# Kernel optimization log

Hardware: AMD Instinct MI355X
Metric: run time of the kernel (lower is better)

Reference implementation:

```python
import jax, jax.numpy as jnp
import numpy as np

N_NODES = 50000
N_EDGES = 800000
NFEAT, NHID, NCLASS = 256, 64, 2


def _deg_norm(idx, n_nodes, dtype):
    deg = jax.ops.segment_sum(jnp.ones(idx.shape[0], dtype=dtype), idx, num_segments=n_nodes)
    return jax.lax.rsqrt(jnp.maximum(deg, 1.0))


def gcn_layer(x, W, b, src, dst, n_nodes):
    # DGL GraphConv, norm='both': h = D_in^{-1/2} * Agg( D_out^{-1/2} * x ) W + b
    # weight applied before aggregation (in_feats >= out_feats path); math-equivalent.
    norm_src = _deg_norm(src, n_nodes, x.dtype)  # out-degree norm of source nodes
    norm_dst = _deg_norm(dst, n_nodes, x.dtype)  # in-degree norm of dest nodes
    h = (x * norm_src[:, None]) @ W              # [N, out]
    agg = jax.ops.segment_sum(h[src], dst, num_segments=n_nodes)  # gather + scatter-add
    return agg * norm_dst[:, None] + b


def setup_inputs() -> dict:
    key = jax.random.key(0)
    k1, k2, k3, k4, k5, k6, k7 = jax.random.split(key, 7)
    x = jax.random.normal(k1, (N_NODES, NFEAT), dtype=jnp.float32)
    src = jax.random.randint(k2, (N_EDGES,), 0, N_NODES, dtype=jnp.int64)
    dst = jax.random.randint(k3, (N_EDGES,), 0, N_NODES, dtype=jnp.int64)
    # Glorot-style init like DGL GraphConv
    W1 = jax.random.normal(k4, (NFEAT, NHID), dtype=jnp.float32) * (2.0 / (NFEAT + NHID)) ** 0.5
    b1 = jnp.zeros((NHID,), dtype=jnp.float32)
    W2 = jax.random.normal(k5, (NHID, NCLASS), dtype=jnp.float32) * (2.0 / (NHID + NCLASS)) ** 0.5
    b2 = jnp.zeros((NCLASS,), dtype=jnp.float32)
    return {"x": x, "src": src, "dst": dst, "W1": W1, "b1": b1, "W2": W2, "b2": b2}


def reference(x, src, dst, W1, b1, W2, b2):
    h = jax.nn.relu(gcn_layer(x, W1, b1, src, dst, N_NODES))
    # dropout=False -> p=0, no-op
    logits = gcn_layer(h, W2, b2, src, dst, N_NODES)
    return jax.nn.log_softmax(logits, axis=1)
```

## Files before the change

kernel.cpp:

```cpp
#include <hip/hip_runtime.h>
#include <math.h>

#define N_NODES 50000
#define N_EDGES 800000
#define NFEAT 256
#define NHID 64
#define NCLASS 2

#define DB 64
#define NDB 782
#define BCAP 1536
#define EPB 2048
#define NB_EDGE ((N_EDGES + EPB - 1) / EPB)
#define CSTRIDE 32

#define OFF_CURD 0
#define OFF_CURS 25024
#define OFF_RBD  50048
#define OFF_NDST 150048
#define OFF_NSRC 200048
#define OFF_W1T  250048
#define OFF_DPK  258240
#define OFF_SV6  1459392
#define OFF_HB   1759680
#define OFF_H2   3359680

typedef __attribute__((ext_vector_type(8))) short bf16x8;
typedef __attribute__((ext_vector_type(4))) float f32x4;

static __device__ __forceinline__ unsigned short f2bf(float f) {
    union { float f; unsigned int u; } v; v.f = f;
    return (unsigned short)((v.u + 0x8000u) >> 16);
}
static __device__ __forceinline__ unsigned int pk2bf(float f0, float f1) {
    union { float f; unsigned int u; } a, b; a.f = f0; b.f = f1;
    return __builtin_amdgcn_perm(b.u + 0x8000u, a.u + 0x8000u, 0x07060302u);
}
static __device__ __forceinline__ float bflo(unsigned int u) {
    union { unsigned int x; float f; } v; v.x = u << 16; return v.f;
}
static __device__ __forceinline__ float bfhi(unsigned int u) {
    union { unsigned int x; float f; } v; v.x = u & 0xffff0000u; return v.f;
}

#define INIT_CUR (2 * NDB * CSTRIDE)
#define INIT_N (INIT_CUR + NFEAT * NHID)
__global__ __launch_bounds__(256) void init_kernel(const float* __restrict__ W1,
                                                   int* __restrict__ cursors,
                                                   unsigned short* __restrict__ w1t) {
    int g = blockIdx.x * 256 + threadIdx.x;
    if (g < INIT_CUR) {
        cursors[g] = 0;
    } else if (g < INIT_N) {
        int idx = g - INIT_CUR;
        int k = idx >> 6, n = idx & 63;
        w1t[n * NFEAT + k] = f2bf(W1[idx]);
    }
}

struct SgShared { int hd[NDB], bd[NDB], cd[NDB], hs[NDB], bs[NDB], cs[NDB]; };
__global__ __launch_bounds__(256) void scatter_kernel(const int* __restrict__ src,
                                                      const int* __restrict__ dst,
                                                      int* __restrict__ cur_d,
                                                      int* __restrict__ cur_s,
                                                      int* __restrict__ dpk,
                                                      unsigned char* __restrict__ sv6) {
    __shared__ SgShared su;
    int t = threadIdx.x;
    for (int i = t; i < NDB; i += 256) { su.hd[i] = 0; su.cd[i] = 0; su.hs[i] = 0; su.cs[i] = 0; }
    __syncthreads();
    int base = blockIdx.x * EPB;
    int ls[8], ld[8];
#pragma unroll
    for (int i = 0; i < 8; ++i) {
        int e = base + t + i * 256;
        ls[i] = (e < N_EDGES) ? src[e] : -1;
        ld[i] = (e < N_EDGES) ? dst[e] : -1;
        if (ld[i] >= 0) {
            atomicAdd(&su.hd[ld[i] >> 6], 1);
            atomicAdd(&su.hs[ls[i] >> 6], 1);
        }
    }
    __syncthreads();
    {
        int i0 = t, i1 = t + 256, i2 = t + 512, i3 = t + 768;
        int hd0 = su.hd[i0], hs0 = su.hs[i0];
        int hd1 = su.hd[i1], hs1 = su.hs[i1];
        int hd2 = su.hd[i2], hs2 = su.hs[i2];
        int hd3 = (i3 < NDB) ? su.hd[i3] : 0;
        int hs3 = (i3 < NDB) ? su.hs[i3] : 0;
        int b0 = 0, b1v = 0, b2v = 0, b3v = 0, c0 = 0, c1v = 0, c2v = 0, c3v = 0;
        if (hd0) b0  = atomicAdd(&cur_d[i0 * CSTRIDE], hd0);
        if (hs0) c0  = atomicAdd(&cur_s[i0 * CSTRIDE], hs0);
        if (hd1) b1v = atomicAdd(&cur_d[i1 * CSTRIDE], hd1);
        if (hs1) c1v = atomicAdd(&cur_s[i1 * CSTRIDE], hs1);
        if (hd2) b2v = atomicAdd(&cur_d[i2 * CSTRIDE], hd2);
        if (hs2) c2v = atomicAdd(&cur_s[i2 * CSTRIDE], hs2);
        if (hd3) b3v = atomicAdd(&cur_d[i3 * CSTRIDE], hd3);
        if (hs3) c3v = atomicAdd(&cur_s[i3 * CSTRIDE], hs3);
        su.bd[i0] = b0;  su.bs[i0] = c0;
        su.bd[i1] = b1v; su.bs[i1] = c1v;
        su.bd[i2] = b2v; su.bs[i2] = c2v;
        if (i3 < NDB) { su.bd[i3] = b3v; su.bs[i3] = c3v; }
    }
    __syncthreads();
#pragma unroll
    for (int i = 0; i < 8; ++i) {
        if (ld[i] >= 0) {
            int bin = ld[i] >> 6;
            int pos = su.bd[bin] + atomicAdd(&su.cd[bin], 1);
            dpk[bin * BCAP + pos] = (ls[i] << 6) | (ld[i] & 63);
            int sbin = ls[i] >> 6;
            int spos = su.bs[sbin] + atomicAdd(&su.cs[sbin], 1);
            sv6[sbin * BCAP + spos] = (unsigned char)(ls[i] & 63);
        }
    }
}

union FinShared {
    struct { int ebuf[BCAP]; int hist4[256]; int hist[64]; int seg[64]; int cur[64]; } d;
    struct { int hist4[256]; } s;
};
__global__ __launch_bounds__(256) void fin_kernel(const int* __restrict__ cur_d,
                                                  const int* __restrict__ cur_s,
                                                  const int* __restrict__ dpk,
                                                  const unsigned char* __restrict__ sv6,
                                                  int2* __restrict__ rbdeg,
                                                  float* __restrict__ norm_dst,
                                                  float* __restrict__ norm_src,
                                                  int* __restrict__ csr) {
    __shared__ FinShared su;
    int t = threadIdx.x;
    int role = blockIdx.x & 1;
    int b = blockIdx.x >> 1;

    if (role == 0) {
        su.s.hist4[t] = 0;
        __syncthreads();
        int cnt = cur_s[b * CSTRIDE];
        int base = b * BCAP;
        int sub = (t & 3) * 64;
        for (int j = t; j < cnt; j += 256) atomicAdd(&su.s.hist4[sub + sv6[base + j]], 1);
        __syncthreads();
        if (t < 64) {
            int gid = b * 64 + t;
            if (gid < N_NODES) {
                int v = su.s.hist4[t] + su.s.hist4[64 + t] + su.s.hist4[128 + t] + su.s.hist4[192 + t];
                norm_src[gid] = rsqrtf(fmaxf((float)v, 1.0f));
            }
        }
    } else {
        int cnt = cur_d[b * CSTRIDE];
        int base = b * BCAP;
        if (t < 64) { su.d.hist[t] = 0; su.d.cur[t] = 0; }
        su.d.hist4[t] = 0;
        for (int j = t; j < cnt; j += 256) su.d.ebuf[j] = dpk[base + j];
        __syncthreads();
        int sub = (t & 3) * 64;
        for (int j = t; j < cnt; j += 256) atomicAdd(&su.d.hist4[sub + (su.d.ebuf[j] & 63)], 1);
        __syncthreads();
        if (t < 64) {
            int v = su.d.hist4[t] + su.d.hist4[64 + t] + su.d.hist4[128 + t] + su.d.hist4[192 + t];
            su.d.hist[t] = v;
            su.d.seg[t] = v;
        }
        __syncthreads();
#pragma unroll
        for (int off = 1; off < 64; off <<= 1) {
            int xv = 0;
            if (t < 64 && t >= off) xv = su.d.seg[t - off];
            __syncthreads();
            if (t < 64) su.d.seg[t] += xv;
            __syncthreads();
        }
        if (t < 64) {
            int v = su.d.hist[t];
            int excl = su.d.seg[t] - v;
            int gid = b * 64 + t;
            if (gid < N_NODES) {
                rbdeg[gid] = make_int2(base + excl, v);
                norm_dst[gid] = rsqrtf(fmaxf((float)v, 1.0f));
            }
            su.d.seg[t] = excl;
        }
        __syncthreads();
        for (int j = t; j < cnt; j += 256) {
            int p = su.d.ebuf[j];
            int dlow = p & 63;
            int pos = base + su.d.seg[dlow] + atomicAdd(&su.d.cur[dlow], 1);
            csr[pos] = ((unsigned)p) >> 6;
        }
    }
}

__global__ __launch_bounds__(128, 3) void gemm_kernel(const float* __restrict__ x,
                                                      const unsigned short* __restrict__ w1t,
                                                      const float* __restrict__ norm_src,
                                                      unsigned short* __restrict__ hb) {
    int t = threadIdx.x;
    int w = t >> 6;
    int l = t & 63;
    int m = l & 15;
    int q = l >> 4;
    int base = (blockIdx.x * 2 + w) * 16;
    if (base >= N_NODES) return;
    const float* xr = &x[(size_t)(base + m) * NFEAT];
    float4 av[16];
#pragma unroll
    for (int i = 0; i < 8; ++i) {
        av[2 * i]     = *(const float4*)(xr + i * 32 + q * 8);
        av[2 * i + 1] = *(const float4*)(xr + i * 32 + q * 8 + 4);
    }
    f32x4 acc[4] = {{0.f, 0.f, 0.f, 0.f}, {0.f, 0.f, 0.f, 0.f},
                    {0.f, 0.f, 0.f, 0.f}, {0.f, 0.f, 0.f, 0.f}};
#pragma unroll
    for (int c8 = 0; c8 < 8; ++c8) {
        int k0 = c8 * 32 + q * 8;
        union { bf16x8 v; unsigned int u[4]; } a;
        a.u[0] = pk2bf(av[2 * c8].x, av[2 * c8].y);
        a.u[1] = pk2bf(av[2 * c8].z, av[2 * c8].w);
        a.u[2] = pk2bf(av[2 * c8 + 1].x, av[2 * c8 + 1].y);
        a.u[3] = pk2bf(av[2 * c8 + 1].z, av[2 * c8 + 1].w);
#pragma unroll
        for (int ct = 0; ct < 4; ++ct) {
            bf16x8 bb = *(const bf16x8*)(&w1t[(ct * 16 + m) * NFEAT + k0]);
            acc[ct] = __builtin_amdgcn_mfma_f32_16x16x32_bf16(a.v, bb, acc[ct], 0, 0, 0);
        }
    }
#pragma unroll
    for (int reg = 0; reg < 4; ++reg) {
        int r = base + q * 4 + reg;
        float ns = norm_src[r];
#pragma unroll
        for (int ct = 0; ct < 4; ++ct)
            hb[(size_t)r * NHID + ct * 16 + m] = f2bf(acc[ct][reg] * ns);
    }
}

__global__ __launch_bounds__(256) void fused1_kernel(const int2* __restrict__ rbdeg,
                                                     const int* __restrict__ csr,
                                                     const unsigned short* __restrict__ hb,
                                                     const float* __restrict__ norm_dst,
                                                     const float* __restrict__ norm_src,
                                                     const float* __restrict__ b1,
                                                     const float* __restrict__ W2,
                                                     float* __restrict__ h2) {
    int gtid = blockIdx.x * blockDim.x + threadIdx.x;
    int node = gtid >> 6;
    int lane = gtid & 63;
    if (node >= N_NODES) return;
    int e8 = lane >> 3, fg = lane & 7;
    int2 rd = rbdeg[node];
    int beg = rd.x;
    int end = beg + rd.y;
    float a0 = 0.f, a1 = 0.f, a2 = 0.f, a3 = 0.f, a4 = 0.f, a5 = 0.f, a6 = 0.f, a7 = 0.f;
    for (int j = beg; j < end; j += 32) {
        int j0 = j + e8, j1 = j0 + 8, j2 = j0 + 16, j3 = j0 + 24;
        uint4 u0 = make_uint4(0u, 0u, 0u, 0u), u1 = make_uint4(0u, 0u, 0u, 0u);
        uint4 u2 = make_uint4(0u, 0u, 0u, 0u), u3 = make_uint4(0u, 0u, 0u, 0u);
        if (j0 < end) u0 = *(const uint4*)(&hb[(size_t)csr[j0] * NHID + fg * 8]);
        if (j1 < end) u1 = *(const uint4*)(&hb[(size_t)csr[j1] * NHID + fg * 8]);
        if (j2 < end) u2 = *(const uint4*)(&hb[(size_t)csr[j2] * NHID + fg * 8]);
        if (j3 < end) u3 = *(const uint4*)(&hb[(size_t)csr[j3] * NHID + fg * 8]);
        a0 += bflo(u0.x) + bflo(u1.x) + bflo(u2.x) + bflo(u3.x);
        a1 += bfhi(u0.x) + bfhi(u1.x) + bfhi(u2.x) + bfhi(u3.x);
        a2 += bflo(u0.y) + bflo(u1.y) + bflo(u2.y) + bflo(u3.y);
        a3 += bfhi(u0.y) + bfhi(u1.y) + bfhi(u2.y) + bfhi(u3.y);
        a4 += bflo(u0.z) + bflo(u1.z) + bflo(u2.z) + bflo(u3.z);
        a5 += bfhi(u0.z) + bfhi(u1.z) + bfhi(u2.z) + bfhi(u3.z);
        a6 += bflo(u0.w) + bflo(u1.w) + bflo(u2.w) + bflo(u3.w);
        a7 += bfhi(u0.w) + bfhi(u1.w) + bfhi(u2.w) + bfhi(u3.w);
    }
#pragma unroll
    for (int off = 8; off <= 32; off <<= 1) {
        a0 += __shfl_xor(a0, off, 64);
        a1 += __shfl_xor(a1, off, 64);
        a2 += __shfl_xor(a2, off, 64);
        a3 += __shfl_xor(a3, off, 64);
        a4 += __shfl_xor(a4, off, 64);
        a5 += __shfl_xor(a5, off, 64);
        a6 += __shfl_xor(a6, off, 64);
        a7 += __shfl_xor(a7, off, 64);
    }
    float nd = norm_dst[node], ns = norm_src[node];
    float4 bv0 = *(const float4*)(&b1[fg * 8]);
    float4 bv1 = *(const float4*)(&b1[fg * 8 + 4]);
    float4 w0 = *(const float4*)(&W2[fg * 16 + 0]);
    float4 w1 = *(const float4*)(&W2[fg * 16 + 4]);
    float4 w2v = *(const float4*)(&W2[fg * 16 + 8]);
    float4 w3 = *(const float4*)(&W2[fg * 16 + 12]);
    float h0 = fmaxf(fmaf(a0, nd, bv0.x), 0.f) * ns;
    float h1 = fmaxf(fmaf(a1, nd, bv0.y), 0.f) * ns;
    float h2f = fmaxf(fmaf(a2, nd, bv0.z), 0.f) * ns;
    float h3 = fmaxf(fmaf(a3, nd, bv0.w), 0.f) * ns;
    float h4 = fmaxf(fmaf(a4, nd, bv1.x), 0.f) * ns;
    float h5 = fmaxf(fmaf(a5, nd, bv1.y), 0.f) * ns;
    float h6 = fmaxf(fmaf(a6, nd, bv1.z), 0.f) * ns;
    float h7 = fmaxf(fmaf(a7, nd, bv1.w), 0.f) * ns;
    float p0 = h0 * w0.x + h1 * w0.z + h2f * w1.x + h3 * w1.z +
               h4 * w2v.x + h5 * w2v.z + h6 * w3.x + h7 * w3.z;
    float p1 = h0 * w0.y + h1 * w0.w + h2f * w1.y + h3 * w1.w +
               h4 * w2v.y + h5 * w2v.w + h6 * w3.y + h7 * w3.w;
#pragma unroll
    for (int off = 1; off <= 4; off <<= 1) {
        p0 += __shfl_xor(p0, off, 64);
        p1 += __shfl_xor(p1, off, 64);
    }
    if (lane == 0) *(float2*)(&h2[node * 2]) = make_float2(p0, p1);
}

__global__ __launch_bounds__(256) void fused2_kernel(const int2* __restrict__ rbdeg,
                                                     const int* __restrict__ csr,
                                                     const float* __restrict__ h2,
                                                     const float* __restrict__ norm_dst,
                                                     const float* __restrict__ b2,
                                                     float* __restrict__ out) {
    int gtid = blockIdx.x * blockDim.x + threadIdx.x;
    int n = gtid >> 4;
    int l16 = gtid & 15;
    if (n >= N_NODES) return;
    int2 rd = rbdeg[n];
    int beg = rd.x, end = rd.x + rd.y;
    float s0 = 0.f, s1 = 0.f;
    for (int j = beg + l16; j < end; j += 16) {
        float2 v = *(const float2*)(&h2[csr[j] * 2]);
        s0 += v.x;
        s1 += v.y;
    }
#pragma unroll
    for (int off = 1; off <= 8; off <<= 1) {
        s0 += __shfl_xor(s0, off, 16);
        s1 += __shfl_xor(s1, off, 16);
    }
    if (l16 == 0) {
        float nd = norm_dst[n];
        float l0 = fmaf(s0, nd, b2[0]);
        float l1 = fmaf(s1, nd, b2[1]);
        float m = fmaxf(l0, l1);
        float lse = m + logf(expf(l0 - m) + expf(l1 - m));
        *(float2*)(&out[n * 2]) = make_float2(l0 - lse, l1 - lse);
    }
}

extern "C" void kernel_launch(void* const* d_in, const int* in_sizes, int n_in,
                              void* d_out, int out_size, void* d_ws, size_t ws_size,
                              hipStream_t stream) {
    const float* x  = (const float*)d_in[0];
    const int* src  = (const int*)d_in[1];
    const int* dst  = (const int*)d_in[2];
    const float* W1 = (const float*)d_in[3];
    const float* b1 = (const float*)d_in[4];
    const float* W2 = (const float*)d_in[5];
    const float* b2 = (const float*)d_in[6];
    float* out = (float*)d_out;
    float* ws  = (float*)d_ws;
    int*   wsi = (int*)d_ws;

    int*   cur_d    = wsi + OFF_CURD;
    int*   cur_s    = wsi + OFF_CURS;
    int2*  rbdeg    = (int2*)(wsi + OFF_RBD);
    float* norm_dst = ws + OFF_NDST;
    float* norm_src = ws + OFF_NSRC;
    unsigned short* w1t = (unsigned short*)(wsi + OFF_W1T);
    int*   dpk      = wsi + OFF_DPK;
    unsigned char* sv6 = (unsigned char*)(wsi + OFF_SV6);
    int*   csr      = wsi + OFF_DPK;
    unsigned short* hb = (unsigned short*)(wsi + OFF_HB);
    float* h2       = ws + OFF_H2;

    init_kernel<<<(INIT_N + 255) / 256, 256, 0, stream>>>(W1, cur_d, w1t);
    scatter_kernel<<<NB_EDGE, 256, 0, stream>>>(src, dst, cur_d, cur_s, dpk, sv6);
    fin_kernel<<<NDB * 2, 256, 0, stream>>>(cur_d, cur_s, dpk, sv6, rbdeg, norm_dst, norm_src, csr);
    {
        int tiles = (N_NODES + 15) / 16;
        gemm_kernel<<<(tiles + 1) / 2, 128, 0, stream>>>(x, w1t, norm_src, hb);
    }
    {
        long long threads = (long long)N_NODES * 64;
        fused1_kernel<<<(int)((threads + 255) / 256), 256, 0, stream>>>(
            rbdeg, csr, hb, norm_dst, norm_src, b1, W2, h2);
    }
    {
        long long threads = (long long)N_NODES * 16;
        fused2_kernel<<<(int)((threads + 255) / 256), 256, 0, stream>>>(
            rbdeg, csr, h2, norm_dst, b2, out);
    }
}
```

Baseline: 196.8 us.

## Replace global atomic bin cursors with per-chunk histograms and a scan

Binning edges no longer relies on global atomicAdd cursors inside the scatter kernel. It now runs in three stages: a seed kernel writes a per-chunk histogram of dst and src bins to global memory (and also converts W1), a scan kernel computes per-chunk base offsets and per-bin counts with wave shuffles, and the scatter kernel reads those bases and writes edges. This removes contended global atomics and makes edge placement deterministic. The cost is an extra kernel launch, a second read of src and dst, and about 2.4 MB of histogram and base traffic.

```diff
diff --git a/kernel.cpp b/kernel.cpp
--- a/kernel.cpp
+++ b/kernel.cpp
@@ -12,18 +12,22 @@
 #define BCAP 1536
 #define EPB 2048
 #define NB_EDGE ((N_EDGES + EPB - 1) / EPB)
-#define CSTRIDE 32
-
-#define OFF_CURD 0
-#define OFF_CURS 25024
-#define OFF_RBD  50048
-#define OFF_NDST 150048
-#define OFF_NSRC 200048
-#define OFF_W1T  250048
-#define OFF_DPK  258240
-#define OFF_SV6  1459392
-#define OFF_HB   1759680
-#define OFF_H2   3359680
+#define HISTW (NB_EDGE * NDB)
+
+#define OFF_CNTD  0
+#define OFF_CNTS  782
+#define OFF_RBD   1564
+#define OFF_NDST  101564
+#define OFF_NSRC  151564
+#define OFF_W1T   201564
+#define OFF_HISTD 209756
+#define OFF_HISTS 515518
+#define OFF_BASED 821280
+#define OFF_BASES 1127042
+#define OFF_DPK   1432804
+#define OFF_SV6   2633956
+#define OFF_HB    2934244
+#define OFF_H2    4534244
 
 typedef __attribute__((ext_vector_type(8))) short bf16x8;
 typedef __attribute__((ext_vector_type(4))) float f32x4;
@@ -43,76 +47,98 @@
     union { unsigned int x; float f; } v; v.x = u & 0xffff0000u; return v.f;
 }
 
-#define INIT_CUR (2 * NDB * CSTRIDE)
-#define INIT_N (INIT_CUR + NFEAT * NHID)
-__global__ __launch_bounds__(256) void init_kernel(const float* __restrict__ W1,
-                                                   int* __restrict__ cursors,
-                                                   unsigned short* __restrict__ w1t) {
-    int g = blockIdx.x * 256 + threadIdx.x;
-    if (g < INIT_CUR) {
-        cursors[g] = 0;
-    } else if (g < INIT_N) {
-        int idx = g - INIT_CUR;
-        int k = idx >> 6, n = idx & 63;
-        w1t[n * NFEAT + k] = f2bf(W1[idx]);
-    }
-}
-
-struct SgShared { int hd[NDB], bd[NDB], cd[NDB], hs[NDB], bs[NDB], cs[NDB]; };
+#define W1T_BLOCKS ((NFEAT * NHID + 255) / 256)
+__global__ __launch_bounds__(256) void seed_kernel(const int* __restrict__ src,
+                                                   const int* __restrict__ dst,
+                                                   const float* __restrict__ W1,
+                                                   unsigned short* __restrict__ w1t,
+                                                   int* __restrict__ histD,
+                                                   int* __restrict__ histS) {
+    int t = threadIdx.x;
+    int bid = blockIdx.x;
+    if (bid < NB_EDGE) {
+        __shared__ int hd[NDB], hs[NDB];
+        for (int i = t; i < NDB; i += 256) { hd[i] = 0; hs[i] = 0; }
+        __syncthreads();
+        int base = bid * EPB;
+#pragma unroll
+        for (int i = 0; i < 8; ++i) {
+            int e = base + t + i * 256;
+            if (e < N_EDGES) {
+                atomicAdd(&hd[dst[e] >> 6], 1);
+                atomicAdd(&hs[src[e] >> 6], 1);
+            }
+        }
+        __syncthreads();
+        for (int i = t; i < NDB; i += 256) {
+            histD[bid * NDB + i] = hd[i];
+            histS[bid * NDB + i] = hs[i];
+        }
+    } else {
+        int idx = (bid - NB_EDGE) * 256 + t;
+        if (idx < NFEAT * NHID) {
+            int k = idx >> 6, n = idx & 63;
+            w1t[n * NFEAT + k] = f2bf(W1[idx]);
+        }
+    }
+}
+
+__global__ __launch_bounds__(64) void scan_kernel(const int* __restrict__ histD,
+                                                  const int* __restrict__ histS,
+                                                  int* __restrict__ baseD,
+                                                  int* __restrict__ baseS,
+                                                  int* __restrict__ cnt_d,
+                                                  int* __restrict__ cnt_s) {
+    int b = blockIdx.x % NDB;
+    int kind = blockIdx.x / NDB;
+    const int* h = kind ? histS : histD;
+    int* bp = kind ? baseS : baseD;
+    int lane = threadIdx.x;
+    int carry = 0;
+    for (int c0 = 0; c0 < NB_EDGE; c0 += 64) {
+        int c = c0 + lane;
+        int v = (c < NB_EDGE) ? h[c * NDB + b] : 0;
+        int inc = v;
+#pragma unroll
+        for (int off = 1; off < 64; off <<= 1) {
+            int u = __shfl_up(inc, off, 64);
+            if (lane >= off) inc += u;
+        }
+        if (c < NB_EDGE) bp[c * NDB + b] = b * BCAP + carry + (inc - v);
+        carry += __shfl(inc, 63, 64);
+    }
+    if (lane == 0) {
+        if (kind) cnt_s[b] = carry; else cnt_d[b] = carry;
+    }
+}
+
 __global__ __launch_bounds__(256) void scatter_kernel(const int* __restrict__ src,
                                                       const int* __restrict__ dst,
-                                                      int* __restrict__ cur_d,
-                                                      int* __restrict__ cur_s,
+                                                      const int* __restrict__ baseD,
+                                                      const int* __restrict__ baseS,
                                                       int* __restrict__ dpk,
                                                       unsigned char* __restrict__ sv6) {
-    __shared__ SgShared su;
+    __shared__ int bd[NDB], bs[NDB], cd[NDB], cs[NDB];
     int t = threadIdx.x;
-    for (int i = t; i < NDB; i += 256) { su.hd[i] = 0; su.cd[i] = 0; su.hs[i] = 0; su.cs[i] = 0; }
+    int chunk = blockIdx.x;
+    for (int i = t; i < NDB; i += 256) {
+        bd[i] = baseD[chunk * NDB + i];
+        bs[i] = baseS[chunk * NDB + i];
+        cd[i] = 0; cs[i] = 0;
+    }
     __syncthreads();
-    int base = blockIdx.x * EPB;
-    int ls[8], ld[8];
+    int base = chunk * EPB;
 #pragma unroll
     for (int i = 0; i < 8; ++i) {
         int e = base + t + i * 256;
-        ls[i] = (e < N_EDGES) ? src[e] : -1;
-        ld[i] = (e < N_EDGES) ? dst[e] : -1;
-        if (ld[i] >= 0) {
-            atomicAdd(&su.hd[ld[i] >> 6], 1);
-            atomicAdd(&su.hs[ls[i] >> 6], 1);
-        }
-    }
-    __syncthreads();
-    {
-        int i0 = t, i1 = t + 256, i2 = t + 512, i3 = t + 768;
-        int hd0 = su.hd[i0], hs0 = su.hs[i0];
-        int hd1 = su.hd[i1], hs1 = su.hs[i1];
-        int hd2 = su.hd[i2], hs2 = su.hs[i2];
-        int hd3 = (i3 < NDB) ? su.hd[i3] : 0;
-        int hs3 = (i3 < NDB) ? su.hs[i3] : 0;
-        int b0 = 0, b1v = 0, b2v = 0, b3v = 0, c0 = 0, c1v = 0, c2v = 0, c3v = 0;
-        if (hd0) b0  = atomicAdd(&cur_d[i0 * CSTRIDE], hd0);
-        if (hs0) c0  = atomicAdd(&cur_s[i0 * CSTRIDE], hs0);
-        if (hd1) b1v = atomicAdd(&cur_d[i1 * CSTRIDE], hd1);
-        if (hs1) c1v = atomicAdd(&cur_s[i1 * CSTRIDE], hs1);
-        if (hd2) b2v = atomicAdd(&cur_d[i2 * CSTRIDE], hd2);
-        if (hs2) c2v = atomicAdd(&cur_s[i2 * CSTRIDE], hs2);
-        if (hd3) b3v = atomicAdd(&cur_d[i3 * CSTRIDE], hd3);
-        if (hs3) c3v = atomicAdd(&cur_s[i3 * CSTRIDE], hs3);
-        su.bd[i0] = b0;  su.bs[i0] = c0;
-        su.bd[i1] = b1v; su.bs[i1] = c1v;
-        su.bd[i2] = b2v; su.bs[i2] = c2v;
-        if (i3 < NDB) { su.bd[i3] = b3v; su.bs[i3] = c3v; }
-    }
-    __syncthreads();
-#pragma unroll
-    for (int i = 0; i < 8; ++i) {
-        if (ld[i] >= 0) {
-            int bin = ld[i] >> 6;
-            int pos = su.bd[bin] + atomicAdd(&su.cd[bin], 1);
-            dpk[bin * BCAP + pos] = (ls[i] << 6) | (ld[i] & 63);
-            int sbin = ls[i] >> 6;
-            int spos = su.bs[sbin] + atomicAdd(&su.cs[sbin], 1);
-            sv6[sbin * BCAP + spos] = (unsigned char)(ls[i] & 63);
+        if (e < N_EDGES) {
+            int s = src[e], d = dst[e];
+            int bin = d >> 6;
+            int pos = bd[bin] + atomicAdd(&cd[bin], 1);
+            dpk[pos] = (s << 6) | (d & 63);
+            int sb = s >> 6;
+            int sp = bs[sb] + atomicAdd(&cs[sb], 1);
+            sv6[sp] = (unsigned char)(s & 63);
         }
     }
 }
@@ -121,8 +147,8 @@
     struct { int ebuf[BCAP]; int hist4[256]; int hist[64]; int seg[64]; int cur[64]; } d;
     struct { int hist4[256]; } s;
 };
-__global__ __launch_bounds__(256) void fin_kernel(const int* __restrict__ cur_d,
-                                                  const int* __restrict__ cur_s,
+__global__ __launch_bounds__(256) void fin_kernel(const int* __restrict__ cnt_d,
+                                                  const int* __restrict__ cnt_s,
                                                   const int* __restrict__ dpk,
                                                   const unsigned char* __restrict__ sv6,
                                                   int2* __restrict__ rbdeg,
@@ -137,7 +163,7 @@
     if (role == 0) {
         su.s.hist4[t] = 0;
         __syncthreads();
-        int cnt = cur_s[b * CSTRIDE];
+        int cnt = cnt_s[b];
         int base = b * BCAP;
         int sub = (t & 3) * 64;
         for (int j = t; j < cnt; j += 256) atomicAdd(&su.s.hist4[sub + sv6[base + j]], 1);
@@ -150,7 +176,7 @@
             }
         }
     } else {
-        int cnt = cur_d[b * CSTRIDE];
+        int cnt = cnt_d[b];
         int base = b * BCAP;
         if (t < 64) { su.d.hist[t] = 0; su.d.cur[t] = 0; }
         su.d.hist4[t] = 0;
@@ -356,21 +382,26 @@
     float* ws  = (float*)d_ws;
     int*   wsi = (int*)d_ws;
 
-    int*   cur_d    = wsi + OFF_CURD;
-    int*   cur_s    = wsi + OFF_CURS;
+    int*   cnt_d    = wsi + OFF_CNTD;
+    int*   cnt_s    = wsi + OFF_CNTS;
     int2*  rbdeg    = (int2*)(wsi + OFF_RBD);
     float* norm_dst = ws + OFF_NDST;
     float* norm_src = ws + OFF_NSRC;
     unsigned short* w1t = (unsigned short*)(wsi + OFF_W1T);
+    int*   histD    = wsi + OFF_HISTD;
+    int*   histS    = wsi + OFF_HISTS;
+    int*   baseD    = wsi + OFF_BASED;
+    int*   baseS    = wsi + OFF_BASES;
     int*   dpk      = wsi + OFF_DPK;
     unsigned char* sv6 = (unsigned char*)(wsi + OFF_SV6);
     int*   csr      = wsi + OFF_DPK;
     unsigned short* hb = (unsigned short*)(wsi + OFF_HB);
     float* h2       = ws + OFF_H2;
 
-    init_kernel<<<(INIT_N + 255) / 256, 256, 0, stream>>>(W1, cur_d, w1t);
-    scatter_kernel<<<NB_EDGE, 256, 0, stream>>>(src, dst, cur_d, cur_s, dpk, sv6);
-    fin_kernel<<<NDB * 2, 256, 0, stream>>>(cur_d, cur_s, dpk, sv6, rbdeg, norm_dst, norm_src, csr);
+    seed_kernel<<<NB_EDGE + W1T_BLOCKS, 256, 0, stream>>>(src, dst, W1, w1t, histD, histS);
+    scan_kernel<<<NDB * 2, 64, 0, stream>>>(histD, histS, baseD, baseS, cnt_d, cnt_s);
+    scatter_kernel<<<NB_EDGE, 256, 0, stream>>>(src, dst, baseD, baseS, dpk, sv6);
+    fin_kernel<<<NDB * 2, 256, 0, stream>>>(cnt_d, cnt_s, dpk, sv6, rbdeg, norm_dst, norm_src, csr);
     {
         int tiles = (N_NODES + 15) / 16;
         gemm_kernel<<<(tiles + 1) / 2, 128, 0, stream>>>(x, w1t, norm_src, hb);
```

Result: faster. 190.4 us (-3.2%).
